# Performance work log

Hardware: AMD Instinct MI355X
Metric: run time of the kernel (lower is better)

## Reference

```python
import jax, jax.numpy as jnp
import numpy as np


def setup_inputs() -> dict:
    key = jax.random.key(0)
    k1, k2, k3 = jax.random.split(key, 3)
    n_nodes, d = 1_000_000, 128
    B, L, w, neg_size = 1024, 80, 5, 4
    A = L - w + 1  # 76 anchors per walk
    walk = jax.random.randint(k1, (B, L), 0, n_nodes)
    # torch.randint(low=1, high=n_nodes-1) -> values in [1, n_nodes-2]
    neg = jax.random.randint(k2, (B, A, neg_size), 1, n_nodes - 1)
    embed = jax.random.normal(k3, (n_nodes, d), dtype=jnp.float32)
    return {"walk": walk, "neg": neg, "embed": embed}


def reference(walk, neg, embed):
    B, L = walk.shape
    A = neg.shape[1]          # L - window_size + 1
    w = L - A + 1             # window_size
    anc = walk[:, :A]                                       # [B, A]
    # pos[b, t, i] = walk[b, t + 1 + i], i in [0, w-2]
    sl = jnp.arange(A)[:, None] + jnp.arange(1, w)[None, :]  # [A, w-1]
    pos = walk[:, sl]                                        # [B, A, w-1]
    e_anc = embed[anc]                                       # [B, A, D]
    # fused gather + per-window dot products
    pos_logit = jnp.einsum('bacd,bad->bac', embed[pos], e_anc)  # [B, A, w-1]
    neg_logit = jnp.einsum('bacd,bad->bac', embed[neg], e_anc)  # [B, A, neg]
    # BCEWithLogitsLoss with labels 1 (pos) and 0 (neg), mean over all elements:
    #   label=1 -> softplus(-x);  label=0 -> softplus(x)
    total = pos_logit.size + neg_logit.size
    loss = (jnp.sum(jax.nn.softplus(-pos_logit)) +
            jnp.sum(jax.nn.softplus(neg_logit))) / total
    return loss
```

## Files before the change

### kernel.cpp

```cpp
#include <hip/hip_runtime.h>
#include <math.h>

#define BD   1024
#define LW   80
#define AA   76
#define NEGS 4
#define D    128
#define PAIRS (BD * AA)
#define WAVES_PER_BLOCK 4
#define PAIRS_PER_WAVE 19
#define NBLOCKS BD

__device__ __forceinline__ float softplus(float x) {
    return fmaxf(x, 0.0f) + log1pf(__expf(-fabsf(x)));
}

__global__ __launch_bounds__(256, 4) void sg_partial(
    const int* __restrict__ walk, const int* __restrict__ neg,
    const float* __restrict__ embed, float* __restrict__ ws)
{
    __shared__ float s_wsum[WAVES_PER_BLOCK];
    const int tid  = threadIdx.x;
    const int lane = tid & 63;
    const int wave = __builtin_amdgcn_readfirstlane(tid >> 6);
    const int b    = blockIdx.x;
    const int a0   = wave * PAIRS_PER_WAVE;

    const float* erow = embed + (size_t)(lane * 2);
    const int*   wrow = walk + b * LW + a0;
    const int*   nrow = neg + (size_t)(b * AA + a0) * NEGS;

    float2 r[5];
    #pragma unroll
    for (int j = 0; j < 5; ++j)
        r[j] = *(const float2*)(erow + (size_t)wrow[j] * D);

    const bool hi1 = lane & 1;
    const bool hi2 = lane & 2;
    const bool hi3 = lane & 4;

    float wsum = 0.0f;

    #pragma unroll
    for (int i = 0; i < PAIRS_PER_WAVE; ++i) {
        const int4 nv = *(const int4*)(nrow + i * NEGS);
        const float2 e4 = *(const float2*)(erow + (size_t)nv.x * D);
        const float2 e5 = *(const float2*)(erow + (size_t)nv.y * D);
        const float2 e6 = *(const float2*)(erow + (size_t)nv.z * D);
        const float2 e7 = *(const float2*)(erow + (size_t)nv.w * D);

        const float2 ea = r[0];
        float a0v = fmaf(ea.x, r[1].x, ea.y * r[1].y);
        float a1v = fmaf(ea.x, r[2].x, ea.y * r[2].y);
        float a2v = fmaf(ea.x, r[3].x, ea.y * r[3].y);
        float a3v = fmaf(ea.x, r[4].x, ea.y * r[4].y);
        float a4v = fmaf(ea.x, e4.x,  ea.y * e4.y);
        float a5v = fmaf(ea.x, e5.x,  ea.y * e5.y);
        float a6v = fmaf(ea.x, e6.x,  ea.y * e6.y);
        float a7v = fmaf(ea.x, e7.x,  ea.y * e7.y);

        float b0 = (hi1 ? a4v : a0v) + __shfl_xor(hi1 ? a0v : a4v, 1);
        float b1 = (hi1 ? a5v : a1v) + __shfl_xor(hi1 ? a1v : a5v, 1);
        float b2 = (hi1 ? a6v : a2v) + __shfl_xor(hi1 ? a2v : a6v, 1);
        float b3 = (hi1 ? a7v : a3v) + __shfl_xor(hi1 ? a3v : a7v, 1);

        float c0 = (hi2 ? b2 : b0) + __shfl_xor(hi2 ? b0 : b2, 2);
        float c1 = (hi2 ? b3 : b1) + __shfl_xor(hi2 ? b1 : b3, 2);

        float dv = (hi3 ? c1 : c0) + __shfl_xor(hi3 ? c0 : c1, 4);
        dv += __shfl_xor(dv, 8);
        dv += __shfl_xor(dv, 16);
        dv += __shfl_xor(dv, 32);
        wsum += softplus(hi1 ? dv : -dv);

        if (i < PAIRS_PER_WAVE - 1) {
            #pragma unroll
            for (int j = 0; j < 4; ++j) r[j] = r[j + 1];
            r[4] = *(const float2*)(erow + (size_t)wrow[i + 5] * D);
        }
    }

    #pragma unroll
    for (int m = 1; m < 64; m <<= 1) wsum += __shfl_xor(wsum, m);

    if (lane == 0) s_wsum[wave] = wsum * 0.125f;
    __syncthreads();
    if (tid == 0)
        ws[blockIdx.x] = s_wsum[0] + s_wsum[1] + s_wsum[2] + s_wsum[3];
}

__global__ __launch_bounds__(256) void sg_reduce(
    const float* __restrict__ ws, float* __restrict__ out)
{
    __shared__ float s[4];
    const int tid = threadIdx.x;
    float sum = 0.0f;
    #pragma unroll
    for (int i = 0; i < NBLOCKS / 256; ++i) sum += ws[tid + i * 256];
    #pragma unroll
    for (int m = 1; m < 64; m <<= 1) sum += __shfl_xor(sum, m);
    const int wave = tid >> 6;
    const int lane = tid & 63;
    if (lane == 0) s[wave] = sum;
    __syncthreads();
    if (tid == 0) {
        const float total = (float)((size_t)PAIRS * 8);
        out[0] = (s[0] + s[1] + s[2] + s[3]) * (1.0f / total);
    }
}

extern "C" void kernel_launch(void* const* d_in, const int* in_sizes, int n_in,
                              void* d_out, int out_size, void* d_ws, size_t ws_size,
                              hipStream_t stream) {
    const int*   walk  = (const int*)d_in[0];
    const int*   neg   = (const int*)d_in[1];
    const float* embed = (const float*)d_in[2];
    float* ws  = (float*)d_ws;
    float* out = (float*)d_out;

    sg_partial<<<NBLOCKS, 256, 0, stream>>>(walk, neg, embed, ws);
    sg_reduce<<<1, 256, 0, stream>>>(ws, out);
}
```

Baseline: 587.7 us.

## Assign one anchor per wave to expose more gather parallelism

Replaces the per-wave sliding window over 19 anchors with one anchor pair per wave, launching about 19x more blocks and raising occupancy hints. This removes the serial chain of dependent gathers within each wave so many more random row loads can be in flight at once. In exchange the anchor and positive rows are re-gathered instead of reused from registers, increasing total memory requests, and the final reduction is widened to handle the larger partial array.

```diff
diff --git a/kernel.cpp b/kernel.cpp
--- a/kernel.cpp
+++ b/kernel.cpp
@@ -8,14 +8,13 @@
 #define D    128
 #define PAIRS (BD * AA)
 #define WAVES_PER_BLOCK 4
-#define PAIRS_PER_WAVE 19
-#define NBLOCKS BD
+#define NBLOCKS (PAIRS / WAVES_PER_BLOCK)
 
 __device__ __forceinline__ float softplus(float x) {
     return fmaxf(x, 0.0f) + log1pf(__expf(-fabsf(x)));
 }
 
-__global__ __launch_bounds__(256, 4) void sg_partial(
+__global__ __launch_bounds__(256, 8) void sg_partial(
     const int* __restrict__ walk, const int* __restrict__ neg,
     const float* __restrict__ embed, float* __restrict__ ws)
 {
@@ -23,80 +22,75 @@
     const int tid  = threadIdx.x;
     const int lane = tid & 63;
     const int wave = __builtin_amdgcn_readfirstlane(tid >> 6);
-    const int b    = blockIdx.x;
-    const int a0   = wave * PAIRS_PER_WAVE;
+    const int p    = blockIdx.x * WAVES_PER_BLOCK + wave;
+    const int b    = p / AA;
+    const int a    = p - b * AA;
+
+    const int* wrow = walk + b * LW + a;
+    const int anc = wrow[0];
+    const int t0  = wrow[1];
+    const int t1  = wrow[2];
+    const int t2  = wrow[3];
+    const int t3  = wrow[4];
+    const int4 nv = *(const int4*)(neg + (size_t)p * NEGS);
 
     const float* erow = embed + (size_t)(lane * 2);
-    const int*   wrow = walk + b * LW + a0;
-    const int*   nrow = neg + (size_t)(b * AA + a0) * NEGS;
+    const float2 ea = *(const float2*)(erow + (size_t)anc  * D);
+    const float2 e0 = *(const float2*)(erow + (size_t)t0   * D);
+    const float2 e1 = *(const float2*)(erow + (size_t)t1   * D);
+    const float2 e2 = *(const float2*)(erow + (size_t)t2   * D);
+    const float2 e3 = *(const float2*)(erow + (size_t)t3   * D);
+    const float2 e4 = *(const float2*)(erow + (size_t)nv.x * D);
+    const float2 e5 = *(const float2*)(erow + (size_t)nv.y * D);
+    const float2 e6 = *(const float2*)(erow + (size_t)nv.z * D);
+    const float2 e7 = *(const float2*)(erow + (size_t)nv.w * D);
 
-    float2 r[5];
-    #pragma unroll
-    for (int j = 0; j < 5; ++j)
-        r[j] = *(const float2*)(erow + (size_t)wrow[j] * D);
+    float a0v = fmaf(ea.x, e0.x, ea.y * e0.y);
+    float a1v = fmaf(ea.x, e1.x, ea.y * e1.y);
+    float a2v = fmaf(ea.x, e2.x, ea.y * e2.y);
+    float a3v = fmaf(ea.x, e3.x, ea.y * e3.y);
+    float a4v = fmaf(ea.x, e4.x, ea.y * e4.y);
+    float a5v = fmaf(ea.x, e5.x, ea.y * e5.y);
+    float a6v = fmaf(ea.x, e6.x, ea.y * e6.y);
+    float a7v = fmaf(ea.x, e7.x, ea.y * e7.y);
 
     const bool hi1 = lane & 1;
     const bool hi2 = lane & 2;
     const bool hi3 = lane & 4;
 
-    float wsum = 0.0f;
+    float b0 = (hi1 ? a4v : a0v) + __shfl_xor(hi1 ? a0v : a4v, 1);
+    float b1 = (hi1 ? a5v : a1v) + __shfl_xor(hi1 ? a1v : a5v, 1);
+    float b2 = (hi1 ? a6v : a2v) + __shfl_xor(hi1 ? a2v : a6v, 1);
+    float b3 = (hi1 ? a7v : a3v) + __shfl_xor(hi1 ? a3v : a7v, 1);
+
+    float c0 = (hi2 ? b2 : b0) + __shfl_xor(hi2 ? b0 : b2, 2);
+    float c1 = (hi2 ? b3 : b1) + __shfl_xor(hi2 ? b1 : b3, 2);
+
+    float dv = (hi3 ? c1 : c0) + __shfl_xor(hi3 ? c0 : c1, 4);
+    dv += __shfl_xor(dv, 8);
+    dv += __shfl_xor(dv, 16);
+    dv += __shfl_xor(dv, 32);
+
+    float v = softplus(hi1 ? dv : -dv);
 
     #pragma unroll
-    for (int i = 0; i < PAIRS_PER_WAVE; ++i) {
-        const int4 nv = *(const int4*)(nrow + i * NEGS);
-        const float2 e4 = *(const float2*)(erow + (size_t)nv.x * D);
-        const float2 e5 = *(const float2*)(erow + (size_t)nv.y * D);
-        const float2 e6 = *(const float2*)(erow + (size_t)nv.z * D);
-        const float2 e7 = *(const float2*)(erow + (size_t)nv.w * D);
+    for (int m = 1; m < 64; m <<= 1) v += __shfl_xor(v, m);
 
-        const float2 ea = r[0];
-        float a0v = fmaf(ea.x, r[1].x, ea.y * r[1].y);
-        float a1v = fmaf(ea.x, r[2].x, ea.y * r[2].y);
-        float a2v = fmaf(ea.x, r[3].x, ea.y * r[3].y);
-        float a3v = fmaf(ea.x, r[4].x, ea.y * r[4].y);
-        float a4v = fmaf(ea.x, e4.x,  ea.y * e4.y);
-        float a5v = fmaf(ea.x, e5.x,  ea.y * e5.y);
-        float a6v = fmaf(ea.x, e6.x,  ea.y * e6.y);
-        float a7v = fmaf(ea.x, e7.x,  ea.y * e7.y);
-
-        float b0 = (hi1 ? a4v : a0v) + __shfl_xor(hi1 ? a0v : a4v, 1);
-        float b1 = (hi1 ? a5v : a1v) + __shfl_xor(hi1 ? a1v : a5v, 1);
-        float b2 = (hi1 ? a6v : a2v) + __shfl_xor(hi1 ? a2v : a6v, 1);
-        float b3 = (hi1 ? a7v : a3v) + __shfl_xor(hi1 ? a3v : a7v, 1);
-
-        float c0 = (hi2 ? b2 : b0) + __shfl_xor(hi2 ? b0 : b2, 2);
-        float c1 = (hi2 ? b3 : b1) + __shfl_xor(hi2 ? b1 : b3, 2);
-
-        float dv = (hi3 ? c1 : c0) + __shfl_xor(hi3 ? c0 : c1, 4);
-        dv += __shfl_xor(dv, 8);
-        dv += __shfl_xor(dv, 16);
-        dv += __shfl_xor(dv, 32);
-        wsum += softplus(hi1 ? dv : -dv);
-
-        if (i < PAIRS_PER_WAVE - 1) {
-            #pragma unroll
-            for (int j = 0; j < 4; ++j) r[j] = r[j + 1];
-            r[4] = *(const float2*)(erow + (size_t)wrow[i + 5] * D);
-        }
-    }
-
-    #pragma unroll
-    for (int m = 1; m < 64; m <<= 1) wsum += __shfl_xor(wsum, m);
-
-    if (lane == 0) s_wsum[wave] = wsum * 0.125f;
+    if (lane == 0) s_wsum[wave] = v * 0.125f;
     __syncthreads();
     if (tid == 0)
         ws[blockIdx.x] = s_wsum[0] + s_wsum[1] + s_wsum[2] + s_wsum[3];
 }
 
-__global__ __launch_bounds__(256) void sg_reduce(
+__global__ __launch_bounds__(1024) void sg_reduce(
     const float* __restrict__ ws, float* __restrict__ out)
 {
-    __shared__ float s[4];
+    __shared__ float s[16];
     const int tid = threadIdx.x;
     float sum = 0.0f;
     #pragma unroll
-    for (int i = 0; i < NBLOCKS / 256; ++i) sum += ws[tid + i * 256];
+    for (int i = 0; i < NBLOCKS / 1024; ++i)
+        sum += ws[tid + i * 1024];
     #pragma unroll
     for (int m = 1; m < 64; m <<= 1) sum += __shfl_xor(sum, m);
     const int wave = tid >> 6;
@@ -104,8 +98,11 @@
     if (lane == 0) s[wave] = sum;
     __syncthreads();
     if (tid == 0) {
+        float acc = 0.0f;
+        #pragma unroll
+        for (int i = 0; i < 16; ++i) acc += s[i];
         const float total = (float)((size_t)PAIRS * 8);
-        out[0] = (s[0] + s[1] + s[2] + s[3]) * (1.0f / total);
+        out[0] = acc * (1.0f / total);
     }
 }
 
@@ -119,5 +116,5 @@
     float* out = (float*)d_out;
 
     sg_partial<<<NBLOCKS, 256, 0, stream>>>(walk, neg, embed, ws);
-    sg_reduce<<<1, 256, 0, stream>>>(ws, out);
+    sg_reduce<<<1, 1024, 0, stream>>>(ws, out);
 }
```

Result: no change. 588.8 us (+0.2%).
